# Kernel tuning notes

Measured on AMD Instinct MI355X. Metric: run time of the kernel, lower is better.

The kernel has to match this reference:

```python
import jax, jax.numpy as jnp
import numpy as np

T, BATCH, DMODEL, H = 2048, 16, 512, 512


def setup_inputs() -> dict:
    key = jax.random.key(0)
    ks = jax.random.split(key, 8)
    x = jax.random.normal(ks[0], (T, BATCH, DMODEL), jnp.float32)
    # initial carry: (lambda=1, h=0) so the concat trick leaves state untouched
    h0_re = jnp.zeros((1, BATCH, H), jnp.float32)
    h0_im = jnp.zeros((1, BATCH, H), jnp.float32)
    # LRU parameterization (Orvieto et al. 2023): |lambda| in [0.9, 0.99]
    u1 = jax.random.uniform(ks[1], (H,), jnp.float32)
    nu_log = jnp.log(-0.5 * jnp.log(u1 * (0.99 ** 2 - 0.9 ** 2) + 0.9 ** 2))
    theta_log = jnp.log(jax.random.uniform(ks[2], (H,), jnp.float32) * (np.pi / 10) + 1e-4)
    B_re = jax.random.normal(ks[3], (H, DMODEL), jnp.float32) / np.sqrt(2 * DMODEL)
    B_im = jax.random.normal(ks[4], (H, DMODEL), jnp.float32) / np.sqrt(2 * DMODEL)
    C_re = jax.random.normal(ks[5], (DMODEL, H), jnp.float32) / np.sqrt(H)
    C_im = jax.random.normal(ks[6], (DMODEL, H), jnp.float32) / np.sqrt(H)
    D_vec = jax.random.normal(ks[7], (DMODEL,), jnp.float32)
    return dict(x=x, h0_re=h0_re, h0_im=h0_im, nu_log=nu_log, theta_log=theta_log,
                B_re=B_re, B_im=B_im, C_re=C_re, C_im=C_im, D_vec=D_vec)


def _binop(qi, qj):
    # associative combine for h_t = a_t * h_{t-1} + b_t
    a_i, b_i = qi
    a_j, b_j = qj
    return (a_j * a_i, a_j * b_i + b_j)


def reference(x, h0_re, h0_im, nu_log, theta_log, B_re, B_im, C_re, C_im, D_vec):
    # diagonal complex recurrence eigenvalues, |Lambda| = exp(-exp(nu_log)) < 1
    Lam = jnp.exp(-jnp.exp(nu_log) + 1j * jnp.exp(theta_log))        # [H] complex64
    gamma = jnp.sqrt(1.0 - jnp.exp(-2.0 * jnp.exp(nu_log)))           # [H]
    Bmat = (B_re + 1j * B_im) * gamma[:, None]                         # [H, D]
    # map_to_h: Bu elements and broadcast Lambda elements
    Bu = jnp.einsum('tbd,hd->tbh', x.astype(jnp.complex64), Bmat)      # [T, B, H]
    Lam_el = jnp.broadcast_to(Lam, Bu.shape)                            # [T, B, H]
    # concat previous state (lambda=1, b=h0) as first scan element
    h0 = (h0_re + 1j * h0_im).astype(jnp.complex64)                    # [1, B, H]
    a = jnp.concatenate([jnp.ones_like(h0), Lam_el], axis=0)          # [T+1, B, H]
    b = jnp.concatenate([h0, Bu], axis=0)                              # [T+1, B, H]
    _, h_all = jax.lax.associative_scan(_binop, (a, b), axis=0)
    h = h_all[1:]                                                       # [T, B, H]
    # map_from_h: y = Re(C h) + D * x (elementwise skip)
    Cmat = C_re + 1j * C_im                                             # [D, H]
    y = jnp.einsum('tbh,dh->tbd', h, Cmat).real + D_vec * x            # [T, B, D]
    final_state = h[-1:]                                                # [1, B, H]
    return (final_state, y)
```

## Files before the change

kernel.cpp:

```cpp
#include <hip/hip_runtime.h>
#include <stdint.h>

typedef short shortx8 __attribute__((ext_vector_type(8)));
typedef float floatx4 __attribute__((ext_vector_type(4)));

#define T_LEN 2048
#define BATCH 16
#define DMODEL 512
#define HDIM 512
#define M_ROWS (T_LEN * BATCH)
#define NCHUNK 32
#define LCHUNK 64
#define NCHAIN (BATCH * HDIM)
#define Y_ELEMS (M_ROWS * DMODEL)

__device__ __forceinline__ unsigned short f2bf(float f) {
    union { float f; unsigned u; } v; v.f = f;
    unsigned r = (v.u + 0x7FFFu + ((v.u >> 16) & 1u)) >> 16;
    return (unsigned short)r;
}
__device__ __forceinline__ float bf2f(unsigned short u) {
    union { unsigned u; float f; } v; v.u = ((unsigned)u) << 16;
    return v.f;
}

__global__ void prep_kernel(const float* __restrict__ nu_log, const float* __restrict__ th_log,
                            float* lam_re, float* lam_im, float* l64_re, float* l64_im, float* gam) {
    int h = blockIdx.x * blockDim.x + threadIdx.x;
    if (h >= HDIM) return;
    double nu  = exp((double)nu_log[h]);
    double th  = exp((double)th_log[h]);
    double mag = exp(-nu);
    double lre = mag * cos(th), lim = mag * sin(th);
    double g   = sqrt(1.0 - exp(-2.0 * nu));
    double zr = lre, zi = lim;
    for (int i = 0; i < 6; ++i) { double nr = zr*zr - zi*zi; zi = 2.0*zr*zi; zr = nr; }
    lam_re[h] = (float)lre; lam_im[h] = (float)lim;
    l64_re[h] = (float)zr;  l64_im[h] = (float)zi;
    gam[h] = (float)g;
}

__global__ void conv_BC_kernel(const float* __restrict__ B_re, const float* __restrict__ B_im,
                               const float* __restrict__ gam,
                               const float* __restrict__ C_re, const float* __restrict__ C_im,
                               unsigned short* __restrict__ Bs, unsigned short* __restrict__ C2) {
    int idx = blockIdx.x * blockDim.x + threadIdx.x;
    if (idx < 524288) {
        int n = idx >> 9;
        int d = idx & 511;
        int h = n & 511;
        float v = (n < HDIM ? B_re[h * DMODEL + d] : B_im[h * DMODEL + d]) * gam[h];
        Bs[idx] = f2bf(v);
    } else {
        int i2 = idx - 524288;
        int d = i2 >> 10;
        int k = i2 & 1023;
        float v = (k < HDIM) ? C_re[d * HDIM + k] : -C_im[d * HDIM + (k - HDIM)];
        C2[i2] = f2bf(v);
    }
}

__global__ void cast_x_kernel(const float4* __restrict__ x4, unsigned short* __restrict__ xb, int n4) {
    int i = blockIdx.x * blockDim.x + threadIdx.x;
    if (i >= n4) return;
    float4 v = x4[i];
    ushort4 u;
    u.x = f2bf(v.x); u.y = f2bf(v.y); u.z = f2bf(v.z); u.w = f2bf(v.w);
    *(ushort4*)(xb + (size_t)i * 4) = u;
}

template <int MODE>
__global__ __launch_bounds__(256, 4) void gemm_nt(const unsigned short* __restrict__ A,
                                                  const unsigned short* __restrict__ Bmat,
                                                  const int K, const int N, const int lgNB,
                                                  unsigned short* __restrict__ OutB,
                                                  float* __restrict__ OutF,
                                                  const float* __restrict__ Dv,
                                                  const unsigned short* __restrict__ Xb) {
    __shared__ unsigned short As[128 * 64];
    __shared__ unsigned short Bs[128 * 64];
    const int L = blockIdx.x;
    const int xcd = L & 7;
    const int slot = L >> 3;
    const int bn = slot & ((1 << lgNB) - 1);
    const int bm = xcd * 32 + (slot >> lgNB);
    const int tid = threadIdx.x;
    const int wv = tid >> 6, lane = tid & 63;
    const int wr = wv >> 1, wc = wv & 1;
    const int lrow = lane & 15, qq = lane >> 4;
    floatx4 acc[4][4] = {};

    const size_t rowA = (size_t)bm * 128, rowB = (size_t)bn * 128;
    for (int k0 = 0; k0 < K; k0 += 64) {
        #pragma unroll
        for (int j = 0; j < 4; ++j) {
            int ch  = j * 256 + wv * 64 + lane;
            int r   = ch >> 3;
            int c16 = ch & 7;
            int g16 = c16 ^ (r & 7);
            const unsigned short* ga = A    + (rowA + r) * (size_t)K + (k0 + g16 * 8);
            const unsigned short* gb = Bmat + (rowB + r) * (size_t)K + (k0 + g16 * 8);
            unsigned short* la = As + (size_t)(j * 256 + wv * 64) * 8;
            unsigned short* lb = Bs + (size_t)(j * 256 + wv * 64) * 8;
            __builtin_amdgcn_global_load_lds((const __attribute__((address_space(1))) void*)ga,
                                             (__attribute__((address_space(3))) void*)la, 16, 0, 0);
            __builtin_amdgcn_global_load_lds((const __attribute__((address_space(1))) void*)gb,
                                             (__attribute__((address_space(3))) void*)lb, 16, 0, 0);
        }
        __syncthreads();
        #pragma unroll
        for (int s = 0; s < 2; ++s) {
            shortx8 af[4], bf[4];
            #pragma unroll
            for (int mi = 0; mi < 4; ++mi) {
                int row = wr * 64 + mi * 16 + lrow;
                int c16 = (s * 4 + qq) ^ (row & 7);
                af[mi] = *(const shortx8*)&As[row * 64 + c16 * 8];
            }
            #pragma unroll
            for (int ni = 0; ni < 4; ++ni) {
                int row = wc * 64 + ni * 16 + lrow;
                int c16 = (s * 4 + qq) ^ (row & 7);
                bf[ni] = *(const shortx8*)&Bs[row * 64 + c16 * 8];
            }
            #pragma unroll
            for (int mi = 0; mi < 4; ++mi)
                #pragma unroll
                for (int ni = 0; ni < 4; ++ni)
                    acc[mi][ni] = __builtin_amdgcn_mfma_f32_16x16x32_bf16(af[mi], bf[ni], acc[mi][ni], 0, 0, 0);
        }
        __syncthreads();
    }

    #pragma unroll
    for (int mi = 0; mi < 4; ++mi) {
        int mbase = bm * 128 + wr * 64 + mi * 16 + qq * 4;
        #pragma unroll
        for (int ni = 0; ni < 4; ++ni) {
            int n = bn * 128 + wc * 64 + ni * 16 + lrow;
            if (MODE == 0) {
                #pragma unroll
                for (int r = 0; r < 4; ++r)
                    OutB[(size_t)(mbase + r) * N + n] = f2bf(acc[mi][ni][r]);
            } else {
                float dv = Dv[n];
                #pragma unroll
                for (int r = 0; r < 4; ++r) {
                    size_t idx = (size_t)(mbase + r) * N + n;
                    OutF[idx] = acc[mi][ni][r] + dv * bf2f(Xb[idx]);
                }
            }
        }
    }
}

__global__ void scan_partial(const unsigned short* __restrict__ Bu,
                             const float* __restrict__ lam_re, const float* __restrict__ lam_im,
                             float* __restrict__ car_re, float* __restrict__ car_im) {
    int gid = blockIdx.x * blockDim.x + threadIdx.x;
    int chunk = gid >> 12;
    int idx = gid & 4095;
    int b = idx >> 8, hp = idx & 255;
    int h = hp * 2;
    float lr0 = lam_re[h], li0 = lam_im[h];
    float lr1 = lam_re[h + 1], li1 = lam_im[h + 1];
    float v0r = 0.f, v0i = 0.f, v1r = 0.f, v1i = 0.f;
    const unsigned short* p = Bu + (size_t)chunk * LCHUNK * BATCH * 1024 + (size_t)b * 1024 + h;
    for (int j = 0; j < LCHUNK; ++j) {
        unsigned rr = *(const unsigned*)p;
        unsigned ii = *(const unsigned*)(p + 512);
        float b0r = bf2f((unsigned short)rr), b1r = bf2f((unsigned short)(rr >> 16));
        float b0i = bf2f((unsigned short)ii), b1i = bf2f((unsigned short)(ii >> 16));
        float n0r = lr0 * v0r - li0 * v0i + b0r;
        float n0i = lr0 * v0i + li0 * v0r + b0i;
        float n1r = lr1 * v1r - li1 * v1i + b1r;
        float n1i = lr1 * v1i + li1 * v1r + b1i;
        v0r = n0r; v0i = n0i; v1r = n1r; v1i = n1i;
        p += BATCH * 1024;
    }
    int c = b * 512 + h;
    *(float2*)&car_re[chunk * NCHAIN + c] = make_float2(v0r, v1r);
    *(float2*)&car_im[chunk * NCHAIN + c] = make_float2(v0i, v1i);
}

__global__ void scan_apply(unsigned short* __restrict__ Bu,
                           const float* __restrict__ lam_re, const float* __restrict__ lam_im,
                           const float* __restrict__ l64_re, const float* __restrict__ l64_im,
                           const float* __restrict__ h0_re, const float* __restrict__ h0_im,
                           const float* __restrict__ car_re, const float* __restrict__ car_im,
                           float* __restrict__ out_final, int interleave) {
    int gid = blockIdx.x * blockDim.x + threadIdx.x;
    int chunk = gid >> 12;
    int idx = gid & 4095;
    int b = idx >> 8, hp = idx & 255;
    int h = hp * 2;
    int c = b * 512 + h;
    float L0r = l64_re[h], L0i = l64_im[h];
    float L1r = l64_re[h + 1], L1i = l64_im[h + 1];
    float v0r = h0_re[c], v0i = h0_im[c];
    float v1r = h0_re[c + 1], v1i = h0_im[c + 1];
    for (int k = 0; k < chunk; ++k) {
        float2 crr = *(const float2*)&car_re[k * NCHAIN + c];
        float2 cii = *(const float2*)&car_im[k * NCHAIN + c];
        float n0r = L0r * v0r - L0i * v0i + crr.x;
        float n0i = L0r * v0i + L0i * v0r + cii.x;
        float n1r = L1r * v1r - L1i * v1i + crr.y;
        float n1i = L1r * v1i + L1i * v1r + cii.y;
        v0r = n0r; v0i = n0i; v1r = n1r; v1i = n1i;
    }
    float lr0 = lam_re[h], li0 = lam_im[h];
    float lr1 = lam_re[h + 1], li1 = lam_im[h + 1];
    unsigned short* p = Bu + (size_t)chunk * LCHUNK * BATCH * 1024 + (size_t)b * 1024 + h;
    for (int j = 0; j < LCHUNK; ++j) {
        unsigned rr = *(const unsigned*)p;
        unsigned ii = *(const unsigned*)(p + 512);
        float b0r = bf2f((unsigned short)rr), b1r = bf2f((unsigned short)(rr >> 16));
        float b0i = bf2f((unsigned short)ii), b1i = bf2f((unsigned short)(ii >> 16));
        float n0r = lr0 * v0r - li0 * v0i + b0r;
        float n0i = lr0 * v0i + li0 * v0r + b0i;
        float n1r = lr1 * v1r - li1 * v1i + b1r;
        float n1i = lr1 * v1i + li1 * v1r + b1i;
        v0r = n0r; v0i = n0i; v1r = n1r; v1i = n1i;
        *(unsigned*)p         = (unsigned)f2bf(v0r) | ((unsigned)f2bf(v1r) << 16);
        *(unsigned*)(p + 512) = (unsigned)f2bf(v0i) | ((unsigned)f2bf(v1i) << 16);
        p += BATCH * 1024;
    }
    if (chunk == NCHUNK - 1) {
        if (interleave) {
            out_final[2 * c]     = v0r;
            out_final[2 * c + 1] = v0i;
            out_final[2 * c + 2] = v1r;
            out_final[2 * c + 3] = v1i;
        } else {
            out_final[c]     = v0r;
            out_final[c + 1] = v1r;
        }
    }
}

extern "C" void kernel_launch(void* const* d_in, const int* in_sizes, int n_in,
                              void* d_out, int out_size, void* d_ws, size_t ws_size,
                              hipStream_t stream) {
    const float* x        = (const float*)d_in[0];
    const float* h0_re    = (const float*)d_in[1];
    const float* h0_im    = (const float*)d_in[2];
    const float* nu_log   = (const float*)d_in[3];
    const float* theta_lg = (const float*)d_in[4];
    const float* B_re     = (const float*)d_in[5];
    const float* B_im     = (const float*)d_in[6];
    const float* C_re     = (const float*)d_in[7];
    const float* C_im     = (const float*)d_in[8];
    const float* D_vec    = (const float*)d_in[9];

    char* ws = (char*)d_ws;
    unsigned short* BuH  = (unsigned short*)(ws + 0);
    unsigned short* xb   = (unsigned short*)(ws + 67108864);
    unsigned short* Bs   = (unsigned short*)(ws + 100663296);
    unsigned short* C2   = (unsigned short*)(ws + 101711872);
    float* car_re        = (float*)(ws + 102760448);
    float* car_im        = (float*)(ws + 103809024);
    float* lam_re        = (float*)(ws + 104857600);
    float* lam_im        = (float*)(ws + 104859648);
    float* l64_re        = (float*)(ws + 104861696);
    float* l64_im        = (float*)(ws + 104863744);
    float* gam           = (float*)(ws + 104865792);

    int fs_elems = out_size - Y_ELEMS;
    int interleave = (fs_elems == 8192) ? 0 : 1;
    if (fs_elems != 8192) fs_elems = 16384;
    float* out_final = (float*)d_out;
    float* y_out     = (float*)d_out + fs_elems;

    prep_kernel<<<2, 256, 0, stream>>>(nu_log, theta_lg, lam_re, lam_im, l64_re, l64_im, gam);
    conv_BC_kernel<<<(1048576) / 256, 256, 0, stream>>>(B_re, B_im, gam, C_re, C_im, Bs, C2);
    cast_x_kernel<<<(Y_ELEMS / 4) / 256, 256, 0, stream>>>((const float4*)x, xb, Y_ELEMS / 4);
    gemm_nt<0><<<2048, 256, 0, stream>>>(xb, Bs, DMODEL, 1024, 3, BuH, nullptr, nullptr, nullptr);
    scan_partial<<<(NCHUNK * NCHAIN / 2) / 256, 256, 0, stream>>>(BuH, lam_re, lam_im, car_re, car_im);
    scan_apply<<<(NCHUNK * NCHAIN / 2) / 256, 256, 0, stream>>>(BuH, lam_re, lam_im, l64_re, l64_im,
                                                                h0_re, h0_im, car_re, car_im,
                                                                out_final, interleave);
    gemm_nt<1><<<1024, 256, 0, stream>>>(BuH, C2, 1024, 512, 2, nullptr, y_out, D_vec, xb);
}
```

Before: 259.4 us.

## Fuse x cast into GEMM, interleave re/im layout, rechunk scan

Removes the separate x-to-bf16 cast kernel: the first GEMM loads fp32 x directly, converts it in registers and stores it to LDS, and the second GEMM reads fp32 x for the skip term. The Bu/hidden layout changes from split real/imag halves to interleaved (re,im) pairs, so each scan thread reads and writes one 16-byte vector covering 4 channels. The scan uses 64 chunks of 32 steps instead of 32 chunks of 64, with lambda^32 carries packed into one interleaved buffer. This trades the cast pass and its bf16 traffic for synchronous, non-async A loads in the GEMM, and the carry-propagation loop in scan_apply is now longer.

```diff
diff --git a/kernel.cpp b/kernel.cpp
--- a/kernel.cpp
+++ b/kernel.cpp
@@ -1,4 +1,5 @@
 #include <hip/hip_runtime.h>
+#include <hip/hip_bf16.h>
 #include <stdint.h>
 
 typedef short shortx8 __attribute__((ext_vector_type(8)));
@@ -9,8 +10,8 @@
 #define DMODEL 512
 #define HDIM 512
 #define M_ROWS (T_LEN * BATCH)
-#define NCHUNK 32
-#define LCHUNK 64
+#define NCHUNK 64
+#define LCHUNK 32
 #define NCHAIN (BATCH * HDIM)
 #define Y_ELEMS (M_ROWS * DMODEL)
 
@@ -23,9 +24,14 @@
     union { unsigned u; float f; } v; v.u = ((unsigned)u) << 16;
     return v.f;
 }
+__device__ __forceinline__ unsigned pk2(float a, float b) {
+    union { __hip_bfloat162 h; unsigned u; } v;
+    v.h = __float22bfloat162_rn(make_float2(a, b));
+    return v.u;
+}
 
 __global__ void prep_kernel(const float* __restrict__ nu_log, const float* __restrict__ th_log,
-                            float* lam_re, float* lam_im, float* l64_re, float* l64_im, float* gam) {
+                            float* lam_re, float* lam_im, float* l32_re, float* l32_im, float* gam) {
     int h = blockIdx.x * blockDim.x + threadIdx.x;
     if (h >= HDIM) return;
     double nu  = exp((double)nu_log[h]);
@@ -34,9 +40,9 @@
     double lre = mag * cos(th), lim = mag * sin(th);
     double g   = sqrt(1.0 - exp(-2.0 * nu));
     double zr = lre, zi = lim;
-    for (int i = 0; i < 6; ++i) { double nr = zr*zr - zi*zi; zi = 2.0*zr*zi; zr = nr; }
+    for (int i = 0; i < 5; ++i) { double nr = zr*zr - zi*zi; zi = 2.0*zr*zi; zr = nr; }
     lam_re[h] = (float)lre; lam_im[h] = (float)lim;
-    l64_re[h] = (float)zr;  l64_im[h] = (float)zi;
+    l32_re[h] = (float)zr;  l32_im[h] = (float)zi;
     gam[h] = (float)g;
 }
 
@@ -48,37 +54,25 @@
     if (idx < 524288) {
         int n = idx >> 9;
         int d = idx & 511;
-        int h = n & 511;
-        float v = (n < HDIM ? B_re[h * DMODEL + d] : B_im[h * DMODEL + d]) * gam[h];
+        int h = n >> 1, pb = n & 1;
+        float v = (pb ? B_im[h * DMODEL + d] : B_re[h * DMODEL + d]) * gam[h];
         Bs[idx] = f2bf(v);
     } else {
         int i2 = idx - 524288;
         int d = i2 >> 10;
         int k = i2 & 1023;
-        float v = (k < HDIM) ? C_re[d * HDIM + k] : -C_im[d * HDIM + (k - HDIM)];
+        int h = k >> 1, pb = k & 1;
+        float v = pb ? -C_im[d * HDIM + h] : C_re[d * HDIM + h];
         C2[i2] = f2bf(v);
     }
 }
 
-__global__ void cast_x_kernel(const float4* __restrict__ x4, unsigned short* __restrict__ xb, int n4) {
-    int i = blockIdx.x * blockDim.x + threadIdx.x;
-    if (i >= n4) return;
-    float4 v = x4[i];
-    ushort4 u;
-    u.x = f2bf(v.x); u.y = f2bf(v.y); u.z = f2bf(v.z); u.w = f2bf(v.w);
-    *(ushort4*)(xb + (size_t)i * 4) = u;
-}
-
-template <int MODE>
-__global__ __launch_bounds__(256, 4) void gemm_nt(const unsigned short* __restrict__ A,
+__global__ __launch_bounds__(256, 4) void gemm_xb(const float* __restrict__ X,
                                                   const unsigned short* __restrict__ Bmat,
-                                                  const int K, const int N, const int lgNB,
-                                                  unsigned short* __restrict__ OutB,
-                                                  float* __restrict__ OutF,
-                                                  const float* __restrict__ Dv,
-                                                  const unsigned short* __restrict__ Xb) {
+                                                  unsigned short* __restrict__ Out) {
+    const int K = 512, N = 1024, lgNB = 3;
     __shared__ unsigned short As[128 * 64];
-    __shared__ unsigned short Bs[128 * 64];
+    __shared__ unsigned short Bsh[128 * 64];
     const int L = blockIdx.x;
     const int xcd = L & 7;
     const int slot = L >> 3;
@@ -98,10 +92,93 @@
             int r   = ch >> 3;
             int c16 = ch & 7;
             int g16 = c16 ^ (r & 7);
-            const unsigned short* ga = A    + (rowA + r) * (size_t)K + (k0 + g16 * 8);
             const unsigned short* gb = Bmat + (rowB + r) * (size_t)K + (k0 + g16 * 8);
-            unsigned short* la = As + (size_t)(j * 256 + wv * 64) * 8;
-            unsigned short* lb = Bs + (size_t)(j * 256 + wv * 64) * 8;
+            unsigned short* lb = Bsh + (size_t)(j * 256 + wv * 64) * 8;
+            __builtin_amdgcn_global_load_lds((const __attribute__((address_space(1))) void*)gb,
+                                             (__attribute__((address_space(3))) void*)lb, 16, 0, 0);
+        }
+        #pragma unroll
+        for (int j = 0; j < 4; ++j) {
+            int ch  = j * 256 + tid;
+            int r   = ch >> 3;
+            int c16 = ch & 7;
+            int g16 = c16 ^ (r & 7);
+            const float* gx = X + (rowA + r) * (size_t)K + (k0 + g16 * 8);
+            float4 a0 = *(const float4*)gx;
+            float4 a1 = *(const float4*)(gx + 4);
+            uint4 w;
+            w.x = pk2(a0.x, a0.y); w.y = pk2(a0.z, a0.w);
+            w.z = pk2(a1.x, a1.y); w.w = pk2(a1.z, a1.w);
+            *(uint4*)&As[(size_t)ch * 8] = w;
+        }
+        __syncthreads();
+        #pragma unroll
+        for (int s = 0; s < 2; ++s) {
+            shortx8 af[4], bf[4];
+            #pragma unroll
+            for (int mi = 0; mi < 4; ++mi) {
+                int row = wr * 64 + mi * 16 + lrow;
+                int c16 = (s * 4 + qq) ^ (row & 7);
+                af[mi] = *(const shortx8*)&As[row * 64 + c16 * 8];
+            }
+            #pragma unroll
+            for (int ni = 0; ni < 4; ++ni) {
+                int row = wc * 64 + ni * 16 + lrow;
+                int c16 = (s * 4 + qq) ^ (row & 7);
+                bf[ni] = *(const shortx8*)&Bsh[row * 64 + c16 * 8];
+            }
+            #pragma unroll
+            for (int mi = 0; mi < 4; ++mi)
+                #pragma unroll
+                for (int ni = 0; ni < 4; ++ni)
+                    acc[mi][ni] = __builtin_amdgcn_mfma_f32_16x16x32_bf16(af[mi], bf[ni], acc[mi][ni], 0, 0, 0);
+        }
+        __syncthreads();
+    }
+    #pragma unroll
+    for (int mi = 0; mi < 4; ++mi) {
+        int mbase = bm * 128 + wr * 64 + mi * 16 + qq * 4;
+        #pragma unroll
+        for (int ni = 0; ni < 4; ++ni) {
+            int n = bn * 128 + wc * 64 + ni * 16 + lrow;
+            #pragma unroll
+            for (int r = 0; r < 4; ++r)
+                Out[(size_t)(mbase + r) * N + n] = f2bf(acc[mi][ni][r]);
+        }
+    }
+}
+
+__global__ __launch_bounds__(256, 4) void gemm_hc(const unsigned short* __restrict__ H2,
+                                                  const unsigned short* __restrict__ C2,
+                                                  const float* __restrict__ X,
+                                                  const float* __restrict__ Dv,
+                                                  float* __restrict__ Y) {
+    const int K = 1024, N = 512, lgNB = 2;
+    __shared__ unsigned short As[128 * 64];
+    __shared__ unsigned short Bsh[128 * 64];
+    const int L = blockIdx.x;
+    const int xcd = L & 7;
+    const int slot = L >> 3;
+    const int bn = slot & ((1 << lgNB) - 1);
+    const int bm = xcd * 32 + (slot >> lgNB);
+    const int tid = threadIdx.x;
+    const int wv = tid >> 6, lane = tid & 63;
+    const int wr = wv >> 1, wc = wv & 1;
+    const int lrow = lane & 15, qq = lane >> 4;
+    floatx4 acc[4][4] = {};
+
+    const size_t rowA = (size_t)bm * 128, rowB = (size_t)bn * 128;
+    for (int k0 = 0; k0 < K; k0 += 64) {
+        #pragma unroll
+        for (int j = 0; j < 4; ++j) {
+            int ch  = j * 256 + wv * 64 + lane;
+            int r   = ch >> 3;
+            int c16 = ch & 7;
+            int g16 = c16 ^ (r & 7);
+            const unsigned short* ga = H2 + (rowA + r) * (size_t)K + (k0 + g16 * 8);
+            const unsigned short* gb = C2 + (rowB + r) * (size_t)K + (k0 + g16 * 8);
+            unsigned short* la = As  + (size_t)(j * 256 + wv * 64) * 8;
+            unsigned short* lb = Bsh + (size_t)(j * 256 + wv * 64) * 8;
             __builtin_amdgcn_global_load_lds((const __attribute__((address_space(1))) void*)ga,
                                              (__attribute__((address_space(3))) void*)la, 16, 0, 0);
             __builtin_amdgcn_global_load_lds((const __attribute__((address_space(1))) void*)gb,
@@ -121,7 +198,7 @@
             for (int ni = 0; ni < 4; ++ni) {
                 int row = wc * 64 + ni * 16 + lrow;
                 int c16 = (s * 4 + qq) ^ (row & 7);
-                bf[ni] = *(const shortx8*)&Bs[row * 64 + c16 * 8];
+                bf[ni] = *(const shortx8*)&Bsh[row * 64 + c16 * 8];
             }
             #pragma unroll
             for (int mi = 0; mi < 4; ++mi)
@@ -131,24 +208,17 @@
         }
         __syncthreads();
     }
-
     #pragma unroll
     for (int mi = 0; mi < 4; ++mi) {
         int mbase = bm * 128 + wr * 64 + mi * 16 + qq * 4;
         #pragma unroll
         for (int ni = 0; ni < 4; ++ni) {
             int n = bn * 128 + wc * 64 + ni * 16 + lrow;
-            if (MODE == 0) {
-                #pragma unroll
-                for (int r = 0; r < 4; ++r)
-                    OutB[(size_t)(mbase + r) * N + n] = f2bf(acc[mi][ni][r]);
-            } else {
-                float dv = Dv[n];
-                #pragma unroll
-                for (int r = 0; r < 4; ++r) {
-                    size_t idx = (size_t)(mbase + r) * N + n;
-                    OutF[idx] = acc[mi][ni][r] + dv * bf2f(Xb[idx]);
-                }
+            float dv = Dv[n];
+            #pragma unroll
+            for (int r = 0; r < 4; ++r) {
+                size_t idx = (size_t)(mbase + r) * N + n;
+                Y[idx] = acc[mi][ni][r] + dv * X[idx];
             }
         }
     }
@@ -156,84 +226,100 @@
 
 __global__ void scan_partial(const unsigned short* __restrict__ Bu,
                              const float* __restrict__ lam_re, const float* __restrict__ lam_im,
-                             float* __restrict__ car_re, float* __restrict__ car_im) {
+                             float* __restrict__ car) {
     int gid = blockIdx.x * blockDim.x + threadIdx.x;
-    int chunk = gid >> 12;
-    int idx = gid & 4095;
-    int b = idx >> 8, hp = idx & 255;
-    int h = hp * 2;
-    float lr0 = lam_re[h], li0 = lam_im[h];
-    float lr1 = lam_re[h + 1], li1 = lam_im[h + 1];
-    float v0r = 0.f, v0i = 0.f, v1r = 0.f, v1i = 0.f;
-    const unsigned short* p = Bu + (size_t)chunk * LCHUNK * BATCH * 1024 + (size_t)b * 1024 + h;
+    int chunk = gid >> 11;
+    int idx = gid & 2047;
+    int b = idx >> 7, q = idx & 127;
+    int h = q * 4;
+    float4 lr4 = *(const float4*)&lam_re[h];
+    float4 li4 = *(const float4*)&lam_im[h];
+    float lrr[4] = {lr4.x, lr4.y, lr4.z, lr4.w};
+    float lii[4] = {li4.x, li4.y, li4.z, li4.w};
+    float vr[4] = {0.f, 0.f, 0.f, 0.f}, vi[4] = {0.f, 0.f, 0.f, 0.f};
+    const unsigned short* p = Bu + (size_t)(chunk * LCHUNK * BATCH + b) * 1024 + q * 8;
     for (int j = 0; j < LCHUNK; ++j) {
-        unsigned rr = *(const unsigned*)p;
-        unsigned ii = *(const unsigned*)(p + 512);
-        float b0r = bf2f((unsigned short)rr), b1r = bf2f((unsigned short)(rr >> 16));
-        float b0i = bf2f((unsigned short)ii), b1i = bf2f((unsigned short)(ii >> 16));
-        float n0r = lr0 * v0r - li0 * v0i + b0r;
-        float n0i = lr0 * v0i + li0 * v0r + b0i;
-        float n1r = lr1 * v1r - li1 * v1i + b1r;
-        float n1i = lr1 * v1i + li1 * v1r + b1i;
-        v0r = n0r; v0i = n0i; v1r = n1r; v1i = n1i;
+        uint4 w = *(const uint4*)p;
+        unsigned wsv[4] = {w.x, w.y, w.z, w.w};
+        #pragma unroll
+        for (int c = 0; c < 4; ++c) {
+            float br = bf2f((unsigned short)wsv[c]);
+            float bi = bf2f((unsigned short)(wsv[c] >> 16));
+            float nr = lrr[c] * vr[c] - lii[c] * vi[c] + br;
+            float ni = lrr[c] * vi[c] + lii[c] * vr[c] + bi;
+            vr[c] = nr; vi[c] = ni;
+        }
         p += BATCH * 1024;
     }
-    int c = b * 512 + h;
-    *(float2*)&car_re[chunk * NCHAIN + c] = make_float2(v0r, v1r);
-    *(float2*)&car_im[chunk * NCHAIN + c] = make_float2(v0i, v1i);
+    float* cp = car + (size_t)(chunk * 2048 + idx) * 8;
+    *(float4*)cp       = make_float4(vr[0], vi[0], vr[1], vi[1]);
+    *(float4*)(cp + 4) = make_float4(vr[2], vi[2], vr[3], vi[3]);
 }
 
 __global__ void scan_apply(unsigned short* __restrict__ Bu,
                            const float* __restrict__ lam_re, const float* __restrict__ lam_im,
-                           const float* __restrict__ l64_re, const float* __restrict__ l64_im,
+                           const float* __restrict__ l32_re, const float* __restrict__ l32_im,
                            const float* __restrict__ h0_re, const float* __restrict__ h0_im,
-                           const float* __restrict__ car_re, const float* __restrict__ car_im,
+                           const float* __restrict__ car,
                            float* __restrict__ out_final, int interleave) {
     int gid = blockIdx.x * blockDim.x + threadIdx.x;
-    int chunk = gid >> 12;
-    int idx = gid & 4095;
-    int b = idx >> 8, hp = idx & 255;
-    int h = hp * 2;
-    int c = b * 512 + h;
-    float L0r = l64_re[h], L0i = l64_im[h];
-    float L1r = l64_re[h + 1], L1i = l64_im[h + 1];
-    float v0r = h0_re[c], v0i = h0_im[c];
-    float v1r = h0_re[c + 1], v1i = h0_im[c + 1];
+    int chunk = gid >> 11;
+    int idx = gid & 2047;
+    int b = idx >> 7, q = idx & 127;
+    int h = q * 4;
+    int c0 = b * 512 + h;
+    float4 Lr4 = *(const float4*)&l32_re[h];
+    float4 Li4 = *(const float4*)&l32_im[h];
+    float Lr[4] = {Lr4.x, Lr4.y, Lr4.z, Lr4.w};
+    float Li[4] = {Li4.x, Li4.y, Li4.z, Li4.w};
+    float4 h0r = *(const float4*)&h0_re[c0];
+    float4 h0i = *(const float4*)&h0_im[c0];
+    float vr[4] = {h0r.x, h0r.y, h0r.z, h0r.w};
+    float vi[4] = {h0i.x, h0i.y, h0i.z, h0i.w};
     for (int k = 0; k < chunk; ++k) {
-        float2 crr = *(const float2*)&car_re[k * NCHAIN + c];
-        float2 cii = *(const float2*)&car_im[k * NCHAIN + c];
-        float n0r = L0r * v0r - L0i * v0i + crr.x;
-        float n0i = L0r * v0i + L0i * v0r + cii.x;
-        float n1r = L1r * v1r - L1i * v1i + crr.y;
-        float n1i = L1r * v1i + L1i * v1r + cii.y;
-        v0r = n0r; v0i = n0i; v1r = n1r; v1i = n1i;
-    }
-    float lr0 = lam_re[h], li0 = lam_im[h];
-    float lr1 = lam_re[h + 1], li1 = lam_im[h + 1];
-    unsigned short* p = Bu + (size_t)chunk * LCHUNK * BATCH * 1024 + (size_t)b * 1024 + h;
+        const float* cp = car + (size_t)(k * 2048 + idx) * 8;
+        float4 a = *(const float4*)cp;
+        float4 bq = *(const float4*)(cp + 4);
+        float cr[4] = {a.x, a.z, bq.x, bq.z};
+        float ci[4] = {a.y, a.w, bq.y, bq.w};
+        #pragma unroll
+        for (int c = 0; c < 4; ++c) {
+            float nr = Lr[c] * vr[c] - Li[c] * vi[c] + cr[c];
+            float ni = Lr[c] * vi[c] + Li[c] * vr[c] + ci[c];
+            vr[c] = nr; vi[c] = ni;
+        }
+    }
+    float4 lr4 = *(const float4*)&lam_re[h];
+    float4 li4 = *(const float4*)&lam_im[h];
+    float lrr[4] = {lr4.x, lr4.y, lr4.z, lr4.w};
+    float lii[4] = {li4.x, li4.y, li4.z, li4.w};
+    unsigned short* p = Bu + (size_t)(chunk * LCHUNK * BATCH + b) * 1024 + q * 8;
     for (int j = 0; j < LCHUNK; ++j) {
-        unsigned rr = *(const unsigned*)p;
-        unsigned ii = *(const unsigned*)(p + 512);
-        float b0r = bf2f((unsigned short)rr), b1r = bf2f((unsigned short)(rr >> 16));
-        float b0i = bf2f((unsigned short)ii), b1i = bf2f((unsigned short)(ii >> 16));
-        float n0r = lr0 * v0r - li0 * v0i + b0r;
-        float n0i = lr0 * v0i + li0 * v0r + b0i;
-        float n1r = lr1 * v1r - li1 * v1i + b1r;
-        float n1i = lr1 * v1i + li1 * v1r + b1i;
-        v0r = n0r; v0i = n0i; v1r = n1r; v1i = n1i;
-        *(unsigned*)p         = (unsigned)f2bf(v0r) | ((unsigned)f2bf(v1r) << 16);
-        *(unsigned*)(p + 512) = (unsigned)f2bf(v0i) | ((unsigned)f2bf(v1i) << 16);
+        uint4 w = *(const uint4*)p;
+        unsigned wsv[4] = {w.x, w.y, w.z, w.w};
+        #pragma unroll
+        for (int c = 0; c < 4; ++c) {
+            float br = bf2f((unsigned short)wsv[c]);
+            float bi = bf2f((unsigned short)(wsv[c] >> 16));
+            float nr = lrr[c] * vr[c] - lii[c] * vi[c] + br;
+            float ni = lrr[c] * vi[c] + lii[c] * vr[c] + bi;
+            vr[c] = nr; vi[c] = ni;
+        }
+        uint4 o;
+        o.x = (unsigned)f2bf(vr[0]) | ((unsigned)f2bf(vi[0]) << 16);
+        o.y = (unsigned)f2bf(vr[1]) | ((unsigned)f2bf(vi[1]) << 16);
+        o.z = (unsigned)f2bf(vr[2]) | ((unsigned)f2bf(vi[2]) << 16);
+        o.w = (unsigned)f2bf(vr[3]) | ((unsigned)f2bf(vi[3]) << 16);
+        *(uint4*)p = o;
         p += BATCH * 1024;
     }
     if (chunk == NCHUNK - 1) {
         if (interleave) {
-            out_final[2 * c]     = v0r;
-            out_final[2 * c + 1] = v0i;
-            out_final[2 * c + 2] = v1r;
-            out_final[2 * c + 3] = v1i;
+            float* o = out_final + (size_t)c0 * 2;
+            *(float4*)o       = make_float4(vr[0], vi[0], vr[1], vi[1]);
+            *(float4*)(o + 4) = make_float4(vr[2], vi[2], vr[3], vi[3]);
         } else {
-            out_final[c]     = v0r;
-            out_final[c + 1] = v1r;
+            *(float4*)&out_final[c0] = make_float4(vr[0], vr[1], vr[2], vr[3]);
         }
     }
 }
@@ -254,16 +340,14 @@
 
     char* ws = (char*)d_ws;
     unsigned short* BuH  = (unsigned short*)(ws + 0);
-    unsigned short* xb   = (unsigned short*)(ws + 67108864);
-    unsigned short* Bs   = (unsigned short*)(ws + 100663296);
-    unsigned short* C2   = (unsigned short*)(ws + 101711872);
-    float* car_re        = (float*)(ws + 102760448);
-    float* car_im        = (float*)(ws + 103809024);
-    float* lam_re        = (float*)(ws + 104857600);
-    float* lam_im        = (float*)(ws + 104859648);
-    float* l64_re        = (float*)(ws + 104861696);
-    float* l64_im        = (float*)(ws + 104863744);
-    float* gam           = (float*)(ws + 104865792);
+    unsigned short* Bs   = (unsigned short*)(ws + 67108864);
+    unsigned short* C2   = (unsigned short*)(ws + 68157440);
+    float* car           = (float*)(ws + 69206016);
+    float* lam_re        = (float*)(ws + 73400320);
+    float* lam_im        = (float*)(ws + 73402368);
+    float* l32_re        = (float*)(ws + 73404416);
+    float* l32_im        = (float*)(ws + 73406464);
+    float* gam           = (float*)(ws + 73408512);
 
     int fs_elems = out_size - Y_ELEMS;
     int interleave = (fs_elems == 8192) ? 0 : 1;
@@ -271,13 +355,11 @@
     float* out_final = (float*)d_out;
     float* y_out     = (float*)d_out + fs_elems;
 
-    prep_kernel<<<2, 256, 0, stream>>>(nu_log, theta_lg, lam_re, lam_im, l64_re, l64_im, gam);
-    conv_BC_kernel<<<(1048576) / 256, 256, 0, stream>>>(B_re, B_im, gam, C_re, C_im, Bs, C2);
-    cast_x_kernel<<<(Y_ELEMS / 4) / 256, 256, 0, stream>>>((const float4*)x, xb, Y_ELEMS / 4);
-    gemm_nt<0><<<2048, 256, 0, stream>>>(xb, Bs, DMODEL, 1024, 3, BuH, nullptr, nullptr, nullptr);
-    scan_partial<<<(NCHUNK * NCHAIN / 2) / 256, 256, 0, stream>>>(BuH, lam_re, lam_im, car_re, car_im);
-    scan_apply<<<(NCHUNK * NCHAIN / 2) / 256, 256, 0, stream>>>(BuH, lam_re, lam_im, l64_re, l64_im,
-                                                                h0_re, h0_im, car_re, car_im,
-                                                                out_final, interleave);
-    gemm_nt<1><<<1024, 256, 0, stream>>>(BuH, C2, 1024, 512, 2, nullptr, y_out, D_vec, xb);
-}
+    prep_kernel<<<2, 256, 0, stream>>>(nu_log, theta_lg, lam_re, lam_im, l32_re, l32_im, gam);
+    conv_BC_kernel<<<4096, 256, 0, stream>>>(B_re, B_im, gam, C_re, C_im, Bs, C2);
+    gemm_xb<<<2048, 256, 0, stream>>>(x, Bs, BuH);
+    scan_partial<<<512, 256, 0, stream>>>(BuH, lam_re, lam_im, car);
+    scan_apply<<<512, 256, 0, stream>>>(BuH, lam_re, lam_im, l32_re, l32_im,
+                                        h0_re, h0_im, car, out_final, interleave);
+    gemm_hc<<<1024, 256, 0, stream>>>(BuH, C2, x, D_vec, y_out);
+}
```

Measured after the change: 279.3 us. 1.08x slower.
